# Performance work log

Measured on AMD Instinct MI355X. Metric: run time of the kernel, lower is better.

Reference implementation:

```python
import jax, jax.numpy as jnp
import numpy as np

N, E, D, L, G = 50000, 1600000, 128, 3, 64


def setup_inputs() -> dict:
    key = jax.random.key(0)
    ks = jax.random.split(key, 10)
    s = 1.0 / np.sqrt(D).astype(np.float32)
    X = jax.random.normal(ks[0], (N, D), jnp.float32)
    edge_index = jax.random.randint(ks[1], (2, E), 0, N, dtype=jnp.int32)
    edge_types = jax.random.randint(ks[2], (E,), 0, 2, dtype=jnp.int32)
    batch_ids = jnp.sort(jax.random.randint(ks[3], (N,), 0, G, dtype=jnp.int32))
    Wd = jax.random.uniform(ks[4], (L, D, D), jnp.float32, -s, s)
    bd = jax.random.uniform(ks[5], (L, D), jnp.float32, -s, s)
    Wc = jax.random.uniform(ks[6], (L, D, D), jnp.float32, -s, s)
    bc = jax.random.uniform(ks[7], (L, D), jnp.float32, -s, s)
    Ws = jax.random.uniform(ks[8], (L, D, D), jnp.float32, -s, s)
    bs = jax.random.uniform(ks[9], (L, D), jnp.float32, -s, s)
    return dict(X=X, Wd=Wd, bd=bd, Wc=Wc, bc=bc, Ws=Ws, bs=bs,
                edge_index=edge_index, edge_types=edge_types, batch_ids=batch_ids)


def reference(X, Wd, bd, Wc, bc, Ws, bs, edge_index, edge_types, batch_ids):
    src, dst = edge_index[0], edge_index[1]
    is_data = (edge_types == 0)[:, None]  # [E,1] edge-type selector
    for l in range(L):
        # Linear commutes with gather: compute node-level GEMMs once,
        # then per-edge gather + type select (same math as per-edge Linear).
        Xd = X @ Wd[l] + bd[l]            # [N,D] data-edge messages
        Xc = X @ Wc[l] + bc[l]            # [N,D] control-edge messages
        msg = jnp.where(is_data, Xd[src], Xc[src])      # [E,D]
        agg = jax.ops.segment_sum(msg, dst, num_segments=N)  # scatter-add
        X = jax.nn.relu(agg + X @ Ws[l] + bs[l])
    # global mean pool per graph
    sums = jax.ops.segment_sum(X, batch_ids, num_segments=G)
    cnts = jax.ops.segment_sum(jnp.ones((N,), X.dtype), batch_ids, num_segments=G)
    return sums / jnp.maximum(cnts, 1.0)[:, None]
```

## Files before the change

kernel.cpp:

```cpp
#include <hip/hip_runtime.h>
#include <hip/hip_fp16.h>

#define N_NODES 50000
#define N_EDGES 1600000
#define DIM     128
#define NLAYERS 3
#define NGRAPHS 64

#define NBUCK   196
#define CSR_BLKS 256
#define EPB     (N_EDGES / CSR_BLKS)
#define EITER   ((EPB + 255) / 256)

#define NSLICE  4
#define SLB     32
#define SLICE_BYTES ((size_t)N_NODES * SLB)

typedef _Float16 half8 __attribute__((ext_vector_type(8)));
typedef float    f32x4 __attribute__((ext_vector_type(4)));
typedef float    f32x2 __attribute__((ext_vector_type(2)));

#define LDK 136

__global__ __launch_bounds__(256) void setup_kernel(
        const float* __restrict__ X, __half* __restrict__ Xh,
        unsigned char* __restrict__ X8,
        const float* __restrict__ Wd, const float* __restrict__ Wc,
        const float* __restrict__ Ws, __half* __restrict__ WT,
        float* __restrict__ sums, int* __restrict__ gcnt) {
    int i = blockIdx.x * 256 + threadIdx.x;
    if (i < N_NODES * DIM / 4) {
        float4 v = *(const float4*)(X + (size_t)i * 4);
        union { __half2 h2[2]; uint2 u; } pk;
        pk.h2[0] = __floats2half2_rn(v.x, v.y);
        pk.h2[1] = __floats2half2_rn(v.z, v.w);
        *(uint2*)(Xh + (size_t)i * 4) = pk.u;
        int q0 = __builtin_amdgcn_cvt_pk_fp8_f32(v.x, v.y, 0, false);
        int q1 = __builtin_amdgcn_cvt_pk_fp8_f32(v.z, v.w, q0, true);
        int n  = i >> 5;
        int j0 = (i & 31) * 4;
        int sl = j0 >> 5;
        int sb = j0 & 31;
        *(unsigned int*)(X8 + sl * SLICE_BYTES + (size_t)n * SLB + sb) =
            (unsigned int)q1;
    }
    if (i < 9 * DIM * DIM) {
        int k  = i & 127;
        int n  = (i >> 7) & 127;
        int lw = i >> 14;
        int l  = lw / 3, w = lw - 3 * l;
        const float* W = ((w == 0) ? Wd : (w == 1) ? Wc : Ws)
                         + (size_t)l * DIM * DIM;
        WT[i] = __float2half(W[k * DIM + n]);
    }
    if (i < NGRAPHS * DIM) sums[i] = 0.f;
    if (i < NGRAPHS) gcnt[i] = 0;
}

__global__ __launch_bounds__(256) void csr1_kernel(const int* __restrict__ dst,
                                                   int* __restrict__ cntmat) {
    __shared__ int hc[NBUCK];
    int tid = threadIdx.x;
    for (int i = tid; i < NBUCK; i += 256) hc[i] = 0;
    __syncthreads();
    int base = blockIdx.x * EPB;
#pragma unroll
    for (int i = 0; i < EITER; ++i) {
        int idx = i * 256 + tid;
        if (idx < EPB) atomicAdd(&hc[dst[base + idx] >> 8], 1);
    }
    __syncthreads();
    for (int i = tid; i < NBUCK; i += 256)
        cntmat[i * CSR_BLKS + blockIdx.x] = hc[i];
}

__global__ __launch_bounds__(256) void scanA_kernel(const int* __restrict__ cntmat,
                                                    int* __restrict__ exc,
                                                    int* __restrict__ btot) {
    __shared__ int sh[256];
    int tid = threadIdx.x, b = blockIdx.x;
    int v = cntmat[b * CSR_BLKS + tid];
    sh[tid] = v;
    __syncthreads();
    for (int o = 1; o < 256; o <<= 1) {
        int t = (tid >= o) ? sh[tid - o] : 0;
        __syncthreads();
        sh[tid] += t;
        __syncthreads();
    }
    exc[b * CSR_BLKS + tid] = sh[tid] - v;
    if (tid == 255) btot[b] = sh[255];
}

__global__ __launch_bounds__(256) void csr2_kernel(const int* __restrict__ src,
                                                   const int* __restrict__ dst,
                                                   const int* __restrict__ et,
                                                   const int* __restrict__ exc,
                                                   const int* __restrict__ btot,
                                                   int* __restrict__ bstart,
                                                   int* __restrict__ esv) {
    __shared__ int sh[256];
    __shared__ int bst[NBUCK];
    __shared__ int cur[NBUCK];
    int tid = threadIdx.x;
    int v = (tid < NBUCK) ? btot[tid] : 0;
    sh[tid] = v;
    __syncthreads();
    for (int o = 1; o < 256; o <<= 1) {
        int t = (tid >= o) ? sh[tid - o] : 0;
        __syncthreads();
        sh[tid] += t;
        __syncthreads();
    }
    if (tid < NBUCK) bst[tid] = sh[tid] - v;
    if (blockIdx.x == 0) {
        if (tid < NBUCK) bstart[tid] = sh[tid] - v;
        if (tid == NBUCK - 1) bstart[NBUCK] = sh[tid];
    }
    __syncthreads();
    if (tid < NBUCK) cur[tid] = exc[tid * CSR_BLKS + blockIdx.x] + bst[tid];
    __syncthreads();
    int base = blockIdx.x * EPB;
#pragma unroll
    for (int i = 0; i < EITER; ++i) {
        int idx = i * 256 + tid;
        if (idx < EPB) {
            int e = base + idx;
            int d = dst[e];
            int pos = atomicAdd(&cur[d >> 8], 1);
            esv[pos] = (src[e] + et[e] * N_NODES) | ((d & 255) << 17);
        }
    }
}

__global__ __launch_bounds__(256) void csr3_kernel(const int* __restrict__ esv,
                                                   const int* __restrict__ bstart,
                                                   unsigned short* __restrict__ col,
                                                   int* __restrict__ row_start,
                                                   int* __restrict__ deg,
                                                   int* __restrict__ degd) {
    __shared__ int cnt[256];
    __shared__ int cntd[256];
    __shared__ int sh[256];
    __shared__ int curD[256];
    __shared__ int curC[256];
    int tid = threadIdx.x, b = blockIdx.x;
    int bs = bstart[b], be = bstart[b + 1];
    cnt[tid] = 0;
    cntd[tid] = 0;
    __syncthreads();
    for (int e = bs + tid; e < be; e += 256) {
        int pk = esv[e];
        int nd = (pk >> 17) & 255;
        atomicAdd(&cnt[nd], 1);
        if ((pk & 0x1FFFF) < N_NODES) atomicAdd(&cntd[nd], 1);
    }
    __syncthreads();
    int v = cnt[tid];
    sh[tid] = v;
    __syncthreads();
    for (int o = 1; o < 256; o <<= 1) {
        int t = (tid >= o) ? sh[tid - o] : 0;
        __syncthreads();
        sh[tid] += t;
        __syncthreads();
    }
    int off  = sh[tid] - v;
    int node = (b << 8) + tid;
    if (node < N_NODES) {
        row_start[node] = bs + off;
        deg[node]       = v;
        degd[node]      = cntd[tid];
    }
    curD[tid] = bs + off;
    curC[tid] = bs + off + cntd[tid];
    __syncthreads();
    for (int e = bs + tid; e < be; e += 256) {
        int pk  = esv[e];
        int nd  = (pk >> 17) & 255;
        int sv  = pk & 0x1FFFF;
        int isC = sv >= N_NODES;
        int pos = atomicAdd(isC ? &curC[nd] : &curD[nd], 1);
        col[pos] = (unsigned short)(sv - (isC ? N_NODES : 0));
    }
}

__device__ __forceinline__ void agg_range(
        const unsigned short* __restrict__ col,
        const unsigned char* __restrict__ Xs,
        unsigned off, int base, int cnt, float* a) {
    if (cnt <= 0) return;
    int last = cnt - 1;
    int nb = (cnt + 7) >> 3;
    int p[8];
#pragma unroll
    for (int i = 0; i < 8; ++i)
        p[i] = col[base + (i < cnt ? i : last)];
    for (int b = 0; b < nb; ++b) {
        int e0 = b * 8;
        uint2 v[8];
#pragma unroll
        for (int i = 0; i < 8; ++i)
            v[i] = *(const uint2*)(Xs + (((unsigned)p[i] * SLB) | off));
        int pn[8];
        if (b + 1 < nb) {
            int e1 = e0 + 8;
#pragma unroll
            for (int i = 0; i < 8; ++i) {
                int idx = e1 + i;
                pn[i] = col[base + (idx < cnt ? idx : last)];
            }
        }
#pragma unroll
        for (int i = 0; i < 8; ++i)
            if (e0 + i >= cnt) { v[i].x = 0u; v[i].y = 0u; }
#pragma unroll
        for (int i = 0; i < 8; ++i) {
            f32x2 f0 = __builtin_amdgcn_cvt_pk_f32_fp8(v[i].x, false);
            f32x2 f1 = __builtin_amdgcn_cvt_pk_f32_fp8(v[i].x, true);
            f32x2 f2 = __builtin_amdgcn_cvt_pk_f32_fp8(v[i].y, false);
            f32x2 f3 = __builtin_amdgcn_cvt_pk_f32_fp8(v[i].y, true);
            a[0] += f0[0]; a[1] += f0[1];
            a[2] += f1[0]; a[3] += f1[1];
            a[4] += f2[0]; a[5] += f2[1];
            a[6] += f3[0]; a[7] += f3[1];
        }
        if (b + 1 < nb) {
#pragma unroll
            for (int i = 0; i < 8; ++i) p[i] = pn[i];
        }
    }
}

__global__ __launch_bounds__(256) void agg_kernel(
        const int* __restrict__ row_start, const int* __restrict__ deg_arr,
        const int* __restrict__ degd_arr,
        const unsigned short* __restrict__ col,
        const unsigned char* __restrict__ X8t,
        __half* __restrict__ Sd, __half* __restrict__ Sc) {
    int b    = blockIdx.x;
    int s    = b & (NSLICE - 1);
    int nb   = b >> 2;
    int tid  = threadIdx.x;
    int nl   = tid >> 2;
    int l4   = tid & 3;
    int node = nb * 64 + nl;
    if (node >= N_NODES) return;

    int rs = row_start[node];
    int dg = deg_arr[node];
    int dd = degd_arr[node];
    const unsigned char* Xs = X8t + (size_t)s * SLICE_BYTES;
    const unsigned off = (unsigned)l4 * 8;

    float aD[8], aC[8];
#pragma unroll
    for (int j = 0; j < 8; ++j) { aD[j] = 0.f; aC[j] = 0.f; }

    agg_range(col, Xs, off, rs, dd, aD);
    agg_range(col, Xs, off, rs + dd, dg - dd, aC);

    union { __half2 h2[4]; uint4 u; } pd, pc;
#pragma unroll
    for (int j = 0; j < 4; ++j) {
        pd.h2[j] = __floats2half2_rn(aD[2 * j], aD[2 * j + 1]);
        pc.h2[j] = __floats2half2_rn(aC[2 * j], aC[2 * j + 1]);
    }
    size_t so = (size_t)node * DIM + s * SLB + l4 * 8;
    *(uint4*)(Sd + so) = pd.u;
    *(uint4*)(Sc + so) = pc.u;
}

__global__ __launch_bounds__(256) void gemm_fused_kernel(
        const __half* __restrict__ Sd, const __half* __restrict__ Sc,
        const __half* __restrict__ Xh,
        const __half* __restrict__ WTl,
        const float* __restrict__ bd, const float* __restrict__ bc,
        const float* __restrict__ bs,
        const int* __restrict__ degd, const int* __restrict__ deg,
        __half* __restrict__ Xh_out, unsigned char* __restrict__ X8_out,
        int write8) {
    __shared__ _Float16 As[64 * LDK];
    __shared__ _Float16 Bs[128 * LDK];

    const int tid = threadIdx.x;
    const int m0  = blockIdx.x * 64;

    const int wv = tid >> 6;
    const int l  = tid & 63;
    const int lm = l & 15;
    const int q  = l >> 4;

    f32x4 acc[4][2];
#pragma unroll
    for (int mt = 0; mt < 4; ++mt) {
        acc[mt][0] = (f32x4){0.f, 0.f, 0.f, 0.f};
        acc[mt][1] = (f32x4){0.f, 0.f, 0.f, 0.f};
    }

    for (int w = 0; w < 3; ++w) {
        if (w) __syncthreads();
        const __half* Asrc = (w == 0) ? Sd : (w == 1) ? Sc : Xh;
#pragma unroll
        for (int i = 0; i < 4; ++i) {
            int c    = i * 256 + tid;
            int row  = c >> 4;
            int colh = (c & 15) * 8;
            uint4 v  = make_uint4(0u, 0u, 0u, 0u);
            int gr   = m0 + row;
            if (gr < N_NODES) v = *(const uint4*)(Asrc + (size_t)gr * DIM + colh);
            *(uint4*)(As + row * LDK + colh) = v;
        }
        {
            const __half* Wt = WTl + (size_t)w * DIM * DIM;
#pragma unroll
            for (int i = 0; i < 8; ++i) {
                int c    = i * 256 + tid;
                int row  = c >> 4;
                int colh = (c & 15) * 8;
                uint4 v = *(const uint4*)(Wt + (size_t)row * DIM + colh);
                *(uint4*)(Bs + row * LDK + colh) = v;
            }
        }
        __syncthreads();

#pragma unroll
        for (int ks = 0; ks < 4; ++ks) {
            int coff = ks * 32 + q * 8;
            half8 am[4];
#pragma unroll
            for (int mt = 0; mt < 4; ++mt)
                am[mt] = *(const half8*)(As + (mt * 16 + lm) * LDK + coff);
            half8 bb0 = *(const half8*)(Bs + (wv * 32 + lm) * LDK + coff);
            half8 bb1 = *(const half8*)(Bs + (wv * 32 + 16 + lm) * LDK + coff);
#pragma unroll
            for (int mt = 0; mt < 4; ++mt) {
                acc[mt][0] = __builtin_amdgcn_mfma_f32_16x16x32_f16(bb0, am[mt], acc[mt][0], 0, 0, 0);
                acc[mt][1] = __builtin_amdgcn_mfma_f32_16x16x32_f16(bb1, am[mt], acc[mt][1], 0, 0, 0);
            }
        }
    }

    const int fb0 = wv * 32 + q * 4;
    const int fb1 = fb0 + 16;
    f32x4 bdv0 = *(const f32x4*)(bd + fb0), bdv1 = *(const f32x4*)(bd + fb1);
    f32x4 bcv0 = *(const f32x4*)(bc + fb0), bcv1 = *(const f32x4*)(bc + fb1);
    f32x4 bsv0 = *(const f32x4*)(bs + fb0), bsv1 = *(const f32x4*)(bs + fb1);
#pragma unroll
    for (int mt = 0; mt < 4; ++mt) {
        int row = m0 + mt * 16 + lm;
        if (row < N_NODES) {
            float dd = (float)degd[row];
            float dc = (float)(deg[row] - degd[row]);
            float v0[4], v1[4];
#pragma unroll
            for (int r = 0; r < 4; ++r) {
                v0[r] = fmaxf(acc[mt][0][r] + dd * bdv0[r] + dc * bcv0[r] + bsv0[r], 0.f);
                v1[r] = fmaxf(acc[mt][1][r] + dd * bdv1[r] + dc * bcv1[r] + bsv1[r], 0.f);
            }
            union { __half2 h2[2]; uint2 u; } p0, p1;
            p0.h2[0] = __floats2half2_rn(v0[0], v0[1]);
            p0.h2[1] = __floats2half2_rn(v0[2], v0[3]);
            p1.h2[0] = __floats2half2_rn(v1[0], v1[1]);
            p1.h2[1] = __floats2half2_rn(v1[2], v1[3]);
            *(uint2*)(Xh_out + (size_t)row * DIM + fb0) = p0.u;
            *(uint2*)(Xh_out + (size_t)row * DIM + fb1) = p1.u;
            if (write8) {
                int q0 = __builtin_amdgcn_cvt_pk_fp8_f32(v0[0], v0[1], 0, false);
                q0 = __builtin_amdgcn_cvt_pk_fp8_f32(v0[2], v0[3], q0, true);
                int q1 = __builtin_amdgcn_cvt_pk_fp8_f32(v1[0], v1[1], 0, false);
                q1 = __builtin_amdgcn_cvt_pk_fp8_f32(v1[2], v1[3], q1, true);
                unsigned char* xb = X8_out + (size_t)wv * SLICE_BYTES
                                  + (size_t)row * SLB;
                *(unsigned int*)(xb + q * 4)      = (unsigned)q0;
                *(unsigned int*)(xb + q * 4 + 16) = (unsigned)q1;
            }
        }
    }
}

__global__ __launch_bounds__(256) void pool_kernel(const __half* __restrict__ X,
                                                   const int* __restrict__ bid,
                                                   float* __restrict__ sums,
                                                   int* __restrict__ gcnt) {
    __shared__ float acc[8][DIM];
    __shared__ int scnt[8];
    __shared__ int sgmin;
    int tid = threadIdx.x;
    for (int i = tid; i < 8 * DIM; i += 256) ((float*)acc)[i] = 0.f;
    if (tid < 8) scnt[tid] = 0;
    int n0 = blockIdx.x * 64;
    if (tid == 0) sgmin = bid[n0];
    __syncthreads();
    int gmin = sgmin;

    int s    = tid >> 5;
    int lane = tid & 31;
    int r0   = n0 + s * 8;

    int g[8];
    union { uint2 u; __half2 h2[2]; } v[8];
#pragma unroll
    for (int i = 0; i < 8; ++i) {
        int r = r0 + i;
        g[i] = (r < N_NODES) ? bid[r] : -1;
    }
#pragma unroll
    for (int i = 0; i < 8; ++i) {
        int r = r0 + i;
        if (r < N_NODES)
            v[i].u = *(const uint2*)(X + (size_t)r * DIM + lane * 4);
        else { v[i].u.x = 0u; v[i].u.y = 0u; }
    }

    float4 a = make_float4(0.f, 0.f, 0.f, 0.f);
    int cur = -1, run = 0;
#pragma unroll
    for (int i = 0; i < 8; ++i) {
        if (g[i] != cur) {
            if (cur >= 0) {
                int slot = cur - gmin;
                if (slot < 8) {
                    atomicAdd(&acc[slot][lane * 4 + 0], a.x);
                    atomicAdd(&acc[slot][lane * 4 + 1], a.y);
                    atomicAdd(&acc[slot][lane * 4 + 2], a.z);
                    atomicAdd(&acc[slot][lane * 4 + 3], a.w);
                    if (lane == 0) atomicAdd(&scnt[slot], run);
                } else {
                    atomicAdd(&sums[cur * DIM + lane * 4 + 0], a.x);
                    atomicAdd(&sums[cur * DIM + lane * 4 + 1], a.y);
                    atomicAdd(&sums[cur * DIM + lane * 4 + 2], a.z);
                    atomicAdd(&sums[cur * DIM + lane * 4 + 3], a.w);
                    if (lane == 0) atomicAdd(&gcnt[cur], run);
                }
            }
            cur = g[i];
            a = make_float4(0.f, 0.f, 0.f, 0.f);
            run = 0;
        }
        if (g[i] >= 0) {
            float2 f0 = __half22float2(v[i].h2[0]);
            float2 f1 = __half22float2(v[i].h2[1]);
            a.x += f0.x; a.y += f0.y; a.z += f1.x; a.w += f1.y;
            run++;
        }
    }
    if (cur >= 0) {
        int slot = cur - gmin;
        if (slot < 8) {
            atomicAdd(&acc[slot][lane * 4 + 0], a.x);
            atomicAdd(&acc[slot][lane * 4 + 1], a.y);
            atomicAdd(&acc[slot][lane * 4 + 2], a.z);
            atomicAdd(&acc[slot][lane * 4 + 3], a.w);
            if (lane == 0) atomicAdd(&scnt[slot], run);
        } else {
            atomicAdd(&sums[cur * DIM + lane * 4 + 0], a.x);
            atomicAdd(&sums[cur * DIM + lane * 4 + 1], a.y);
            atomicAdd(&sums[cur * DIM + lane * 4 + 2], a.z);
            atomicAdd(&sums[cur * DIM + lane * 4 + 3], a.w);
            if (lane == 0) atomicAdd(&gcnt[cur], run);
        }
    }
    __syncthreads();

    for (int slot = 0; slot < 8; ++slot) {
        if (scnt[slot] > 0) {
            int gg = gmin + slot;
            for (int i = tid; i < DIM; i += 256)
                atomicAdd(&sums[gg * DIM + i], acc[slot][i]);
            if (tid == 0) atomicAdd(&gcnt[gg], scnt[slot]);
        }
    }
}

__global__ __launch_bounds__(256) void div_kernel(const float* __restrict__ sums,
                                                  const int* __restrict__ gcnt,
                                                  float* __restrict__ out) {
    int i = blockIdx.x * 256 + threadIdx.x;
    if (i < NGRAPHS * DIM) {
        int g = i >> 7;
        out[i] = sums[i] / fmaxf((float)gcnt[g], 1.f);
    }
}

extern "C" void kernel_launch(void* const* d_in, const int* in_sizes, int n_in,
                              void* d_out, int out_size, void* d_ws, size_t ws_size,
                              hipStream_t stream) {
    const float* Xin = (const float*)d_in[0];
    const float* Wd  = (const float*)d_in[1];
    const float* bd  = (const float*)d_in[2];
    const float* Wc  = (const float*)d_in[3];
    const float* bc  = (const float*)d_in[4];
    const float* Ws  = (const float*)d_in[5];
    const float* bs  = (const float*)d_in[6];
    const int* edge_index = (const int*)d_in[7];
    const int* edge_types = (const int*)d_in[8];
    const int* batch_ids  = (const int*)d_in[9];

    const int* src = edge_index;
    const int* dst = edge_index + N_EDGES;

    const size_t NBH = (size_t)N_NODES * DIM * sizeof(__half);
    const size_t NB8 = (size_t)N_NODES * DIM;
    char* w = (char*)d_ws;
    auto take = [&](size_t bytes) {
        char* p = w;
        w += (bytes + 255) & ~(size_t)255;
        return p;
    };
    __half* Xh0  = (__half*)take(NBH);
    __half* Xh1  = (__half*)take(NBH);
    unsigned char* X8a = (unsigned char*)take(NB8);
    unsigned char* X8b = (unsigned char*)take(NB8);
    __half* SdB  = (__half*)take(NBH);
    __half* ScB  = (__half*)take(NBH);
    __half* WT   = (__half*)take((size_t)9 * DIM * DIM * sizeof(__half));
    unsigned short* col = (unsigned short*)take((size_t)N_EDGES * 2);
    int* esv     = (int*)take((size_t)N_EDGES * 4);
    int* cntmat  = (int*)take((size_t)NBUCK * CSR_BLKS * 4);
    int* exc     = (int*)take((size_t)NBUCK * CSR_BLKS * 4);
    int* btot    = (int*)take((size_t)NBUCK * 4);
    int* bstart  = (int*)take((size_t)(NBUCK + 1) * 4);
    int* rowst   = (int*)take((size_t)N_NODES * 4);
    int* deg     = (int*)take((size_t)N_NODES * 4);
    int* degd    = (int*)take((size_t)N_NODES * 4);
    float* sums  = (float*)take((size_t)NGRAPHS * DIM * 4);
    int* gcnt    = (int*)take(NGRAPHS * 4);

    setup_kernel<<<(N_NODES * DIM / 4 + 255) / 256, 256, 0, stream>>>(
        Xin, Xh0, X8a, Wd, Wc, Ws, WT, sums, gcnt);

    csr1_kernel<<<CSR_BLKS, 256, 0, stream>>>(dst, cntmat);
    scanA_kernel<<<NBUCK, 256, 0, stream>>>(cntmat, exc, btot);
    csr2_kernel<<<CSR_BLKS, 256, 0, stream>>>(src, dst, edge_types, exc,
                                              btot, bstart, esv);
    csr3_kernel<<<NBUCK, 256, 0, stream>>>(esv, bstart, col, rowst, deg, degd);

    const int GEMM_MBLK = (N_NODES + 63) / 64;
    const int AGG_BLKS  = ((N_NODES + 63) / 64) * NSLICE;

    const __half*      Xhc = Xh0;
    const unsigned char* X8c = X8a;
    __half*            XhN[3] = {Xh1, Xh0, Xh1};
    unsigned char*     X8N[3] = {X8b, X8a, X8b};
    for (int l = 0; l < NLAYERS; ++l) {
        agg_kernel<<<AGG_BLKS, 256, 0, stream>>>(rowst, deg, degd, col, X8c,
                                                 SdB, ScB);
        gemm_fused_kernel<<<GEMM_MBLK, 256, 0, stream>>>(
            SdB, ScB, Xhc, WT + (size_t)l * 3 * DIM * DIM,
            bd + (size_t)l * DIM, bc + (size_t)l * DIM, bs + (size_t)l * DIM,
            degd, deg, XhN[l], X8N[l], (l < NLAYERS - 1) ? 1 : 0);
        Xhc = XhN[l];
        X8c = X8N[l];
    }

    const int POOL_BLKS = (N_NODES + 63) / 64;
    pool_kernel<<<POOL_BLKS, 256, 0, stream>>>(Xhc, batch_ids, sums, gcnt);
    div_kernel<<<(NGRAPHS * DIM + 255) / 256, 256, 0, stream>>>(sums, gcnt,
                                                                (float*)d_out);
}
```

Before: 337.6 us.

## Prefetch next GEMM operand tiles into registers and shrink aggregation blocks

The fused GEMM now loads the next A/W tile pair (Sc/Xh and the next weight slice) into registers while MFMAs run on the current LDS tile, then stores it to LDS between barriers. This overlaps global-load latency with compute. Separately, the aggregation kernel uses 128-thread blocks covering 32 nodes instead of 256 threads covering 64, which doubles the block count to improve load balance across CUs. The prefetch adds register pressure from 12 uint4 values per thread, which could reduce occupancy.

```diff
diff --git a/kernel.cpp b/kernel.cpp
--- a/kernel.cpp
+++ b/kernel.cpp
@@ -232,7 +232,7 @@
     }
 }
 
-__global__ __launch_bounds__(256) void agg_kernel(
+__global__ __launch_bounds__(128) void agg_kernel(
         const int* __restrict__ row_start, const int* __restrict__ deg_arr,
         const int* __restrict__ degd_arr,
         const unsigned short* __restrict__ col,
@@ -244,7 +244,7 @@
     int tid  = threadIdx.x;
     int nl   = tid >> 2;
     int l4   = tid & 3;
-    int node = nb * 64 + nl;
+    int node = nb * 32 + nl;
     if (node >= N_NODES) return;
 
     int rs = row_start[node];
@@ -291,6 +291,10 @@
     const int lm = l & 15;
     const int q  = l >> 4;
 
+    const int arow[4] = { (0 * 256 + tid) >> 4, (1 * 256 + tid) >> 4,
+                          (2 * 256 + tid) >> 4, (3 * 256 + tid) >> 4 };
+    const int acol = (tid & 15) * 8;
+
     f32x4 acc[4][2];
 #pragma unroll
     for (int mt = 0; mt < 4; ++mt) {
@@ -298,31 +302,49 @@
         acc[mt][1] = (f32x4){0.f, 0.f, 0.f, 0.f};
     }
 
+    {
+        uint4 a0[4], b0[8];
+#pragma unroll
+        for (int i = 0; i < 4; ++i) {
+            int gr = m0 + arow[i];
+            a0[i] = make_uint4(0u, 0u, 0u, 0u);
+            if (gr < N_NODES) a0[i] = *(const uint4*)(Sd + (size_t)gr * DIM + acol);
+        }
+#pragma unroll
+        for (int i = 0; i < 8; ++i) {
+            int c = i * 256 + tid;
+            b0[i] = *(const uint4*)(WTl + (size_t)(c >> 4) * DIM + (c & 15) * 8);
+        }
+#pragma unroll
+        for (int i = 0; i < 4; ++i)
+            *(uint4*)(As + arow[i] * LDK + acol) = a0[i];
+#pragma unroll
+        for (int i = 0; i < 8; ++i) {
+            int c = i * 256 + tid;
+            *(uint4*)(Bs + (c >> 4) * LDK + (c & 15) * 8) = b0[i];
+        }
+    }
+    __syncthreads();
+
+#pragma unroll
     for (int w = 0; w < 3; ++w) {
-        if (w) __syncthreads();
-        const __half* Asrc = (w == 0) ? Sd : (w == 1) ? Sc : Xh;
-#pragma unroll
-        for (int i = 0; i < 4; ++i) {
-            int c    = i * 256 + tid;
-            int row  = c >> 4;
-            int colh = (c & 15) * 8;
-            uint4 v  = make_uint4(0u, 0u, 0u, 0u);
-            int gr   = m0 + row;
-            if (gr < N_NODES) v = *(const uint4*)(Asrc + (size_t)gr * DIM + colh);
-            *(uint4*)(As + row * LDK + colh) = v;
-        }
-        {
-            const __half* Wt = WTl + (size_t)w * DIM * DIM;
+        uint4 a_pf[4], b_pf[8];
+        if (w < 2) {
+            const __half* An = (w == 0) ? Sc : Xh;
+#pragma unroll
+            for (int i = 0; i < 4; ++i) {
+                int gr = m0 + arow[i];
+                a_pf[i] = make_uint4(0u, 0u, 0u, 0u);
+                if (gr < N_NODES)
+                    a_pf[i] = *(const uint4*)(An + (size_t)gr * DIM + acol);
+            }
+            const __half* Wn = WTl + (size_t)(w + 1) * DIM * DIM;
 #pragma unroll
             for (int i = 0; i < 8; ++i) {
-                int c    = i * 256 + tid;
-                int row  = c >> 4;
-                int colh = (c & 15) * 8;
-                uint4 v = *(const uint4*)(Wt + (size_t)row * DIM + colh);
-                *(uint4*)(Bs + row * LDK + colh) = v;
-            }
-        }
-        __syncthreads();
+                int c = i * 256 + tid;
+                b_pf[i] = *(const uint4*)(Wn + (size_t)(c >> 4) * DIM + (c & 15) * 8);
+            }
+        }
 
 #pragma unroll
         for (int ks = 0; ks < 4; ++ks) {
@@ -338,6 +360,19 @@
                 acc[mt][0] = __builtin_amdgcn_mfma_f32_16x16x32_f16(bb0, am[mt], acc[mt][0], 0, 0, 0);
                 acc[mt][1] = __builtin_amdgcn_mfma_f32_16x16x32_f16(bb1, am[mt], acc[mt][1], 0, 0, 0);
             }
+        }
+
+        if (w < 2) {
+            __syncthreads();
+#pragma unroll
+            for (int i = 0; i < 4; ++i)
+                *(uint4*)(As + arow[i] * LDK + acol) = a_pf[i];
+#pragma unroll
+            for (int i = 0; i < 8; ++i) {
+                int c = i * 256 + tid;
+                *(uint4*)(Bs + (c >> 4) * LDK + (c & 15) * 8) = b_pf[i];
+            }
+            __syncthreads();
         }
     }
 
@@ -537,14 +572,14 @@
     csr3_kernel<<<NBUCK, 256, 0, stream>>>(esv, bstart, col, rowst, deg, degd);
 
     const int GEMM_MBLK = (N_NODES + 63) / 64;
-    const int AGG_BLKS  = ((N_NODES + 63) / 64) * NSLICE;
+    const int AGG_BLKS  = ((N_NODES + 31) / 32) * NSLICE;
 
     const __half*      Xhc = Xh0;
     const unsigned char* X8c = X8a;
     __half*            XhN[3] = {Xh1, Xh0, Xh1};
     unsigned char*     X8N[3] = {X8b, X8a, X8b};
     for (int l = 0; l < NLAYERS; ++l) {
-        agg_kernel<<<AGG_BLKS, 256, 0, stream>>>(rowst, deg, degd, col, X8c,
+        agg_kernel<<<AGG_BLKS, 128, 0, stream>>>(rowst, deg, degd, col, X8c,
                                                  SdB, ScB);
         gemm_fused_kernel<<<GEMM_MBLK, 256, 0, stream>>>(
             SdB, ScB, Xhc, WT + (size_t)l * 3 * DIM * DIM,
```

Result: slower. 385.1 us (+14.1%).
